# Kernel optimization log

Hardware: AMD Instinct MI355X
Metric: run time of the kernel (lower is better)

## Reference

```python
import jax, jax.numpy as jnp
import numpy as np

B = 1048576
S = 8
K = 10  # n_facts
EPS = 1e-8
ENTROPY_W = 0.01
DIVERSITY_W = 0.1


def setup_inputs() -> dict:
    key = jax.random.key(0)
    k1, k2, k3, k4, k5 = jax.random.split(key, 5)
    p = jax.random.uniform(k1, (B, 2, K), dtype=jnp.float32) + 1e-3
    pCS = p / jnp.sum(p, axis=-1, keepdims=True)  # normalized probs like Categorical
    base_loss = jax.random.uniform(k2, (1,), dtype=jnp.float32)
    Y = jax.random.randint(k3, (B,), 0, 19, dtype=jnp.int32)
    samples1 = jax.random.randint(k4, (S, B), 0, K, dtype=jnp.int32)
    samples2 = jax.random.randint(k5, (S, B), 0, K, dtype=jnp.int32)
    return {"pCS": pCS, "base_loss": base_loss, "Y": Y,
            "samples1": samples1, "samples2": samples2}


def reference(pCS, base_loss, Y, samples1, samples2):
    n_facts = pCS.shape[-1]
    s = samples1.shape[0]
    p1 = pCS[:, 0, :]  # [B, K]
    p2 = pCS[:, 1, :]
    # entropy regularization
    ent1 = -jnp.sum(p1 * jnp.log(p1 + EPS), axis=-1).mean()
    ent2 = -jnp.sum(p2 * jnp.log(p2 + EPS), axis=-1).mean()
    entropy_loss = -(ent1 + ent2) / 2
    # diversity: count unique (d1,d2) pairs per batch element (vectorized bincount-style)
    pairs = (samples1 * n_facts + samples2).T  # [B, S]
    eq = pairs[:, :, None] == pairs[:, None, :]  # [B, S, S]
    earlier = jnp.tril(jnp.ones((s, s), dtype=bool), k=-1)  # j < i
    dup = jnp.any(eq & earlier[None], axis=-1)  # [B, S] True if seen before
    unique_counts = jnp.sum(~dup, axis=-1).astype(jnp.float32)  # [B]
    diversity = unique_counts.mean()
    max_diversity = min(s, n_facts * n_facts)
    diversity_ratio = diversity / max_diversity
    diversity_loss = -jnp.log(diversity_ratio + EPS)
    # REINFORCE leave-one-out (computed, not added to total in original)
    pred_labels = samples1 + samples2  # [S, B] (addition task)
    correct = (pred_labels == Y[None, :]).astype(jnp.float32)
    sample_acc = correct.mean()
    b_idx = jnp.arange(p1.shape[0])[None, :]
    log_probs = jnp.log(p1)[b_idx, samples1] + jnp.log(p2)[b_idx, samples2]  # [S, B]
    baseline = (jnp.sum(correct, axis=0, keepdims=True) - correct) / (s - 1 + EPS)
    advantage = jax.lax.stop_gradient(correct - baseline)
    rloo_loss = -jnp.mean(log_probs * advantage)
    total_loss = base_loss[0] + ENTROPY_W * entropy_loss + DIVERSITY_W * diversity_loss
    return jnp.stack([total_loss, rloo_loss, diversity_loss, sample_acc])
```

## Files before the change

kernel.cpp:

```cpp
#include <hip/hip_runtime.h>

#define S_CONST 8
#define K_CONST 10
#define EPSF 1e-8f
#define ROWS 256

__global__ __launch_bounds__(256) void fml_reduce(
        const float* __restrict__ pCS,
        const int* __restrict__ Y,
        const int* __restrict__ s1g,
        const int* __restrict__ s2g,
        double* __restrict__ partials,
        int B)
{
    __shared__ float sp[ROWS * 20];
    __shared__ float red[4][4];

    float ent = 0.f, uniq = 0.f, corr = 0.f, rloo = 0.f;
    const int tid = threadIdx.x;
    const int ntiles = (B + ROWS - 1) / ROWS;

    for (int tile = blockIdx.x; tile < ntiles; tile += gridDim.x) {
        const int base = tile * ROWS;

        const float4* src = reinterpret_cast<const float4*>(pCS + (size_t)base * 20);
        float4* dst = reinterpret_cast<float4*>(sp);
        const bool full = (base + ROWS) <= B;
        #pragma unroll
        for (int k = 0; k < 5; ++k) {
            const int g = tid + (k << 8);
            float4 v = make_float4(1.f, 1.f, 1.f, 1.f);
            if (full || (base + g / 5) < B) v = src[g];
            ent += v.x * __logf(v.x) + v.y * __logf(v.y)
                 + v.z * __logf(v.z) + v.w * __logf(v.w);
            dst[g] = v;
        }
        __syncthreads();

        const int row = base + tid;
        if (row < B) {
            const int y = Y[row];

            int a1[S_CONST], a2[S_CONST], pr[S_CONST];
            float c[S_CONST];
            float csum = 0.f;
            #pragma unroll
            for (int s = 0; s < S_CONST; ++s) {
                a1[s] = s1g[(size_t)s * B + row];
                a2[s] = s2g[(size_t)s * B + row];
                pr[s] = a1[s] * K_CONST + a2[s];
                c[s]  = (a1[s] + a2[s] == y) ? 1.f : 0.f;
                csum += c[s];
            }
            corr += csum;

            #pragma unroll
            for (int i = 0; i < S_CONST; ++i) {
                bool dup = false;
                #pragma unroll
                for (int j = 0; j < i; ++j) dup = dup || (pr[i] == pr[j]);
                uniq += dup ? 0.f : 1.f;
            }

            const float* my = &sp[tid * 20];
            #pragma unroll
            for (int s = 0; s < S_CONST; ++s) {
                const float g1 = my[a1[s]];
                const float g2 = my[10 + a2[s]];
                const float adv = c[s] - (csum - c[s]) / 7.0f;
                rloo += __logf(g1 * g2) * adv;
            }
        }
        __syncthreads();
    }

    #pragma unroll
    for (int off = 32; off >= 1; off >>= 1) {
        ent  += __shfl_xor(ent,  off);
        uniq += __shfl_xor(uniq, off);
        corr += __shfl_xor(corr, off);
        rloo += __shfl_xor(rloo, off);
    }

    const int lane = threadIdx.x & 63;
    const int wave = threadIdx.x >> 6;
    if (lane == 0) {
        red[wave][0] = ent; red[wave][1] = uniq;
        red[wave][2] = corr; red[wave][3] = rloo;
    }
    __syncthreads();
    if (threadIdx.x == 0) {
        double e = 0, u = 0, cs = 0, rl = 0;
        #pragma unroll
        for (int w = 0; w < 4; ++w) {
            e += (double)red[w][0]; u += (double)red[w][1];
            cs += (double)red[w][2]; rl += (double)red[w][3];
        }
        double* p = &partials[(size_t)blockIdx.x * 4];
        p[0] = e; p[1] = u; p[2] = cs; p[3] = rl;
    }
}

__global__ __launch_bounds__(1024) void fml_finalize(
        const double* __restrict__ partials,
        const float* __restrict__ base_loss,
        float* __restrict__ out, int B, int nblocks)
{
    __shared__ double red[16][4];
    double e = 0, u = 0, cs = 0, rl = 0;
    for (int i = threadIdx.x; i < nblocks; i += 1024) {
        const double* p = &partials[(size_t)i * 4];
        e += p[0]; u += p[1]; cs += p[2]; rl += p[3];
    }
    #pragma unroll
    for (int off = 32; off >= 1; off >>= 1) {
        e  += __shfl_xor(e,  off);
        u  += __shfl_xor(u,  off);
        cs += __shfl_xor(cs, off);
        rl += __shfl_xor(rl, off);
    }
    const int lane = threadIdx.x & 63;
    const int wave = threadIdx.x >> 6;
    if (lane == 0) { red[wave][0] = e; red[wave][1] = u; red[wave][2] = cs; red[wave][3] = rl; }
    __syncthreads();
    if (threadIdx.x == 0) {
        e = 0; u = 0; cs = 0; rl = 0;
        #pragma unroll
        for (int w = 0; w < 16; ++w) {
            e += red[w][0]; u += red[w][1]; cs += red[w][2]; rl += red[w][3];
        }
        const double dB = (double)B;
        const float entropy_loss = (float)(e / (2.0 * dB));
        const float diversity = (float)(u / dB);
        const float ratio = diversity / 8.0f;
        const float diversity_loss = -logf(ratio + EPSF);
        const float sample_acc = (float)(cs / (dB * (double)S_CONST));
        const float rloo_loss  = (float)(-rl / (dB * (double)S_CONST));
        out[0] = base_loss[0] + 0.01f * entropy_loss + 0.1f * diversity_loss;
        out[1] = rloo_loss;
        out[2] = diversity_loss;
        out[3] = sample_acc;
    }
}

extern "C" void kernel_launch(void* const* d_in, const int* in_sizes, int n_in,
                              void* d_out, int out_size, void* d_ws, size_t ws_size,
                              hipStream_t stream) {
    const float* pCS       = (const float*)d_in[0];
    const float* base_loss = (const float*)d_in[1];
    const int*   Y         = (const int*)d_in[2];
    const int*   s1        = (const int*)d_in[3];
    const int*   s2        = (const int*)d_in[4];
    float* out = (float*)d_out;
    const int B = in_sizes[2];

    double* partials = (double*)d_ws;

    const int block = 256;
    const int grid = 2048;
    fml_reduce<<<grid, block, 0, stream>>>(pCS, Y, s1, s2, partials, B);
    fml_finalize<<<1, 1024, 0, stream>>>(partials, base_loss, out, B, grid);
}
```

Before: 42.72 us.

## Give each wave its own 64-row chunk and replace block barriers with wave barriers

Work is now split so that each wavefront owns a 64-row chunk with its own shared-memory slice. This lets the block-wide __syncthreads be replaced by wave-level barriers. The sample and label loads are also issued before the pCS tile load so their latency can overlap. The aim is to remove block-wide stalls in a memory-bound streaming reduction. It relies on wave-level ordering being enough for LDS visibility within a wavefront, and it shrinks the granularity of each contiguous pCS read.

```diff
diff --git a/kernel.cpp b/kernel.cpp
--- a/kernel.cpp
+++ b/kernel.cpp
@@ -3,7 +3,6 @@
 #define S_CONST 8
 #define K_CONST 10
 #define EPSF 1e-8f
-#define ROWS 256
 
 __global__ __launch_bounds__(256) void fml_reduce(
         const float* __restrict__ pCS,
@@ -13,41 +12,57 @@
         double* __restrict__ partials,
         int B)
 {
-    __shared__ float sp[ROWS * 20];
+    __shared__ float sp[4][64 * 20];
     __shared__ float red[4][4];
 
+    const int lane = threadIdx.x & 63;
+    const int wv   = threadIdx.x >> 6;
+    float* sw = sp[wv];
+
     float ent = 0.f, uniq = 0.f, corr = 0.f, rloo = 0.f;
-    const int tid = threadIdx.x;
-    const int ntiles = (B + ROWS - 1) / ROWS;
 
-    for (int tile = blockIdx.x; tile < ntiles; tile += gridDim.x) {
-        const int base = tile * ROWS;
+    const int nchunks = (B + 63) >> 6;
+    const int gwaves  = gridDim.x << 2;
+    for (int ch = (blockIdx.x << 2) + wv; ch < nchunks; ch += gwaves) {
+        const int base = ch << 6;
+        const int row  = base + lane;
+        const bool full = (base + 64) <= B;
+        const bool inb  = full || (row < B);
+
+        int y = 0;
+        int a1[S_CONST], a2[S_CONST];
+        if (inb) {
+            y = Y[row];
+            #pragma unroll
+            for (int s = 0; s < S_CONST; ++s) {
+                a1[s] = s1g[(size_t)s * B + row];
+                a2[s] = s2g[(size_t)s * B + row];
+            }
+        } else {
+            y = -1;
+            #pragma unroll
+            for (int s = 0; s < S_CONST; ++s) { a1[s] = 0; a2[s] = 0; }
+        }
 
         const float4* src = reinterpret_cast<const float4*>(pCS + (size_t)base * 20);
-        float4* dst = reinterpret_cast<float4*>(sp);
-        const bool full = (base + ROWS) <= B;
+        float4* dst = reinterpret_cast<float4*>(sw);
         #pragma unroll
         for (int k = 0; k < 5; ++k) {
-            const int g = tid + (k << 8);
+            const int g = lane + (k << 6);
             float4 v = make_float4(1.f, 1.f, 1.f, 1.f);
             if (full || (base + g / 5) < B) v = src[g];
             ent += v.x * __logf(v.x) + v.y * __logf(v.y)
                  + v.z * __logf(v.z) + v.w * __logf(v.w);
             dst[g] = v;
         }
-        __syncthreads();
+        __builtin_amdgcn_wave_barrier();
 
-        const int row = base + tid;
-        if (row < B) {
-            const int y = Y[row];
-
-            int a1[S_CONST], a2[S_CONST], pr[S_CONST];
+        if (inb) {
+            int pr[S_CONST];
             float c[S_CONST];
             float csum = 0.f;
             #pragma unroll
             for (int s = 0; s < S_CONST; ++s) {
-                a1[s] = s1g[(size_t)s * B + row];
-                a2[s] = s2g[(size_t)s * B + row];
                 pr[s] = a1[s] * K_CONST + a2[s];
                 c[s]  = (a1[s] + a2[s] == y) ? 1.f : 0.f;
                 csum += c[s];
@@ -62,7 +77,7 @@
                 uniq += dup ? 0.f : 1.f;
             }
 
-            const float* my = &sp[tid * 20];
+            const float* my = &sw[lane * 20];
             #pragma unroll
             for (int s = 0; s < S_CONST; ++s) {
                 const float g1 = my[a1[s]];
@@ -71,7 +86,7 @@
                 rloo += __logf(g1 * g2) * adv;
             }
         }
-        __syncthreads();
+        __builtin_amdgcn_wave_barrier();
     }
 
     #pragma unroll
@@ -82,11 +97,9 @@
         rloo += __shfl_xor(rloo, off);
     }
 
-    const int lane = threadIdx.x & 63;
-    const int wave = threadIdx.x >> 6;
     if (lane == 0) {
-        red[wave][0] = ent; red[wave][1] = uniq;
-        red[wave][2] = corr; red[wave][3] = rloo;
+        red[wv][0] = ent; red[wv][1] = uniq;
+        red[wv][2] = corr; red[wv][3] = rloo;
     }
     __syncthreads();
     if (threadIdx.x == 0) {
```

After: 38.15 us. 10.7% less time.
